# Optimization experiments

Hardware: AMD Instinct MI355X
Metric: run time of the kernel (lower is better)

The kernel has to match this reference:

```python
import jax, jax.numpy as jnp
import numpy as np

N = 50000      # nodes
D = 256        # hid_size (span_emb_size)
DH = D // 2    # per-direction GNN output
V = 2          # num_views = len(retypes)
E = 800000     # edges per view per direction (avg degree 16)


def _gnn(x, edges, W, b):
    """Mean-aggregation GCN message passing: h_dst = relu(mean_{src->dst} x_src @ W + b)."""
    src, dst = edges[0], edges[1]
    msg = x[src] @ W                                   # [E, DH] gather + GEMM
    agg = jax.ops.segment_sum(msg, dst, num_segments=N)
    deg = jax.ops.segment_sum(jnp.ones((msg.shape[0],), x.dtype), dst, num_segments=N)
    return jax.nn.relu(agg / jnp.maximum(deg, 1.0)[:, None] + b)


def setup_inputs() -> dict:
    key = jax.random.key(0)
    ks = jax.random.split(key, 10)
    inps = jax.random.normal(ks[0], (N, D), dtype=jnp.float32)
    fw_edges = jax.random.randint(ks[1], (V, 2, E), 0, N, dtype=jnp.int32)
    bw_edges = jax.random.randint(ks[2], (V, 2, E), 0, N, dtype=jnp.int32)
    s = 1.0 / np.sqrt(D)
    W_fw = jax.random.uniform(ks[3], (V, D, DH), jnp.float32, -s, s)
    b_fw = jax.random.uniform(ks[4], (V, DH), jnp.float32, -s, s)
    W_bw = jax.random.uniform(ks[5], (V, D, DH), jnp.float32, -s, s)
    b_bw = jax.random.uniform(ks[6], (V, DH), jnp.float32, -s, s)
    W1 = jax.random.uniform(ks[7], (D, D), jnp.float32, -s, s)
    b1 = jax.random.uniform(ks[8], (D,), jnp.float32, -s, s)
    return {"inps": inps, "fw_edges": fw_edges, "bw_edges": bw_edges,
            "W_fw": W_fw, "b_fw": b_fw, "W_bw": W_bw, "b_bw": b_bw,
            "W1": W1, "b1": b1}


def reference(inps, fw_edges, bw_edges, W_fw, b_fw, W_bw, b_bw, W1, b1):
    # dropout is identity at inference (p applied only in training)
    acc = jnp.zeros_like(inps)
    for v in range(V):  # small fixed number of structurally distinct views
        fw_o = _gnn(inps, fw_edges[v], W_fw[v], b_fw[v])   # [N, DH]
        bw_o = _gnn(inps, bw_edges[v], W_bw[v], b_bw[v])   # [N, DH]
        acc = acc + jnp.concatenate([bw_o, fw_o], axis=-1)  # [N, D], summed over views
    feats = jax.nn.relu(acc) @ W1 + b1 + inps               # act -> linear1 -> residual
    return feats
```

## Files before the change

kernel.cpp:

```cpp
#include <hip/hip_runtime.h>

#define D_ 256
#define DH_ 128
#define NBMAX 128
#define BCAP 9216

using bf16x8 = __attribute__((ext_vector_type(8))) short;
using f32x4  = __attribute__((ext_vector_type(4))) float;
using f32x2  = __attribute__((ext_vector_type(2))) float;

__device__ __forceinline__ unsigned short f2bf(float f) {
  unsigned int u = __builtin_bit_cast(unsigned int, f);
  u += 0x7fffu + ((u >> 16) & 1u);
  return (unsigned short)(u >> 16);
}
__device__ __forceinline__ unsigned char f2fp8(float f) {
  unsigned int pk = __builtin_amdgcn_cvt_pk_fp8_f32(f, 0.f, 0u, false);
  return (unsigned char)(pk & 0xffu);
}


__global__ __launch_bounds__(512) void part_k(const int* __restrict__ fw,
                                              const int* __restrict__ bw,
                                              int* __restrict__ gcnt,
                                              unsigned int* __restrict__ buckets,
                                              int E_, int nb) {
  __shared__ int hist[NBMAX];
  __shared__ int gbase[NBMAX];
  int g = blockIdx.y;
  const int* src = (g < 2 ? fw : bw) + (size_t)(g & 1) * 2 * E_;
  const int* dst = src + E_;
  int t = threadIdx.x;
  for (int i = t; i < nb; i += 512) hist[i] = 0;
  __syncthreads();
  int base = blockIdx.x * 8192;
  unsigned int pk[16];
  int lp[16];
#pragma unroll
  for (int j = 0; j < 16; ++j) {
    int e = base + j * 512 + t;
    if (e < E_) {
      int s = src[e], d = dst[e];
      pk[j] = (unsigned int)s | ((unsigned int)d << 16);
      lp[j] = atomicAdd(&hist[d >> 9], 1);
    } else {
      pk[j] = 0u; lp[j] = -1;
    }
  }
  __syncthreads();
  for (int i = t; i < nb; i += 512) gbase[i] = atomicAdd(&gcnt[g * NBMAX + i], hist[i]);
  __syncthreads();
#pragma unroll
  for (int j = 0; j < 16; ++j) {
    if (lp[j] >= 0) {
      int b = pk[j] >> 25;
      int pos = gbase[b] + lp[j];
      if (pos < BCAP) buckets[((size_t)(g * NBMAX + b)) * BCAP + pos] = pk[j];
    }
  }
}

__global__ __launch_bounds__(256) void csr_k(const unsigned int* __restrict__ buckets,
                                             const int* __restrict__ gcnt,
                                             int* __restrict__ deg, int* __restrict__ offs,
                                             int* __restrict__ csr, int N_, int E_) {
  __shared__ int ldeg[512];
  __shared__ int loff[512];
  __shared__ int wsum[4];
  __shared__ int red[4];
  int g = blockIdx.y, b = blockIdx.x;
  int t = threadIdx.x;
  int lane = t & 63, w = t >> 6;
  int cnt = min(gcnt[g * NBMAX + b], BCAP);
  const unsigned int* ebuf = buckets + ((size_t)(g * NBMAX + b)) * BCAP;
  int nodebase = b << 9;
  int nloc = min(512, N_ - nodebase);
  for (int i = t; i < 512; i += 256) ldeg[i] = 0;
  int val = (t < b) ? min(gcnt[g * NBMAX + t], BCAP) : 0;
  for (int o = 1; o < 64; o <<= 1) val += __shfl_xor(val, o, 64);
  if (lane == 0) red[w] = val;
  __syncthreads();
  int gb = red[0] + red[1] + red[2] + red[3];
  for (int i = t; i < cnt; i += 256) atomicAdd(&ldeg[(ebuf[i] >> 16) & 511], 1);
  __syncthreads();
  int i0 = w * 128 + lane * 2;
  int a0 = ldeg[i0], a1 = ldeg[i0 + 1];
  int pair = a0 + a1, incl = pair;
  for (int o = 1; o < 64; o <<= 1) {
    int x = __shfl_up(incl, o, 64);
    if (lane >= o) incl += x;
  }
  if (lane == 63) wsum[w] = incl;
  __syncthreads();
  int wpre = 0;
  for (int k = 0; k < w; ++k) wpre += wsum[k];
  int e0 = wpre + incl - pair;
  loff[i0] = e0;
  loff[i0 + 1] = e0 + a0;
  __syncthreads();
  for (int i = t; i < nloc; i += 256) {
    deg[(size_t)g * N_ + nodebase + i] = ldeg[i];
    offs[(size_t)g * N_ + nodebase + i] = gb + loff[i];
  }
  for (int i = t; i < 512; i += 256) ldeg[i] = 0;
  __syncthreads();
  int* csrg = csr + (size_t)g * E_ + gb;
  for (int i = t; i < cnt; i += 256) {
    unsigned int pk = ebuf[i];
    int d = (pk >> 16) & 511;
    int lp = atomicAdd(&ldeg[d], 1);
    csrg[loff[d] + lp] = (int)(pk & 0xffffu);
  }
}


__global__ void prepw_k(const float* __restrict__ Wfw, const float* __restrict__ Wbw,
                        const float* __restrict__ W1,
                        unsigned short* __restrict__ Wt, unsigned short* __restrict__ W1t,
                        int* __restrict__ gcnt) {
  int i = blockIdx.x * blockDim.x + threadIdx.x;
  if (i < 4 * NBMAX) gcnt[i] = 0;
  const int nw = 4 * D_ * DH_;
  if (i < nw) {
    int g = i >> 15;
    int r = i & 32767;
    int n = r >> 8, k = r & 255;
    const float* W = (g < 2 ? Wfw : Wbw) + (size_t)(g & 1) * D_ * DH_;
    Wt[i] = f2bf(W[k * DH_ + n]);
  } else if (i < nw + D_ * D_) {
    int r = i - nw;
    int c = r >> 8, k = r & 255;
    W1t[r] = f2bf(W1[k * D_ + c]);
  }
}


__global__ __launch_bounds__(512, 4) void ygemm_k(const float* __restrict__ x,
                                                  const unsigned short* __restrict__ Wt,
                                                  unsigned char* __restrict__ y, int N_) {
  __shared__ unsigned short At[64 * 256];
  int t = threadIdx.x, lane = t & 63, w = t >> 6;
  int tile = blockIdx.x;
#pragma unroll
  for (int it = 0; it < 8; ++it) {
    int idx = it * 512 + t;
    int row = idx >> 6, slot = idx & 63;
    int gr = tile * 64 + row;
    float4 v = {0.f, 0.f, 0.f, 0.f};
    if (gr < N_) v = ((const float4*)x)[(size_t)gr * 64 + slot];
    int c = slot * 4;
    int sc2 = (c & 7) | ((((c >> 3)) ^ (row & 7)) << 3);
    ushort4 o;
    o.x = f2bf(v.x); o.y = f2bf(v.y); o.z = f2bf(v.z); o.w = f2bf(v.w);
    *(ushort4*)&At[row * 256 + sc2] = o;
  }
  __syncthreads();
  int krow = (lane >> 4) * 8;
  int l15 = lane & 15;
  int g = w >> 1, ch = w & 1;
  const unsigned short* Wg = Wt + (size_t)g * (DH_ * D_);
  f32x4 acc[4][4];
#pragma unroll
  for (int a = 0; a < 4; ++a)
#pragma unroll
    for (int b = 0; b < 4; ++b) acc[a][b] = (f32x4){0.f, 0.f, 0.f, 0.f};
#pragma unroll
  for (int kk = 0; kk < 8; ++kk) {
    bf16x8 bfr[4];
#pragma unroll
    for (int ct = 0; ct < 4; ++ct) {
      int n = ch * 64 + ct * 16 + l15;
      bfr[ct] = *(const bf16x8*)(Wg + (size_t)n * 256 + kk * 32 + krow);
    }
    bf16x8 afr[4];
#pragma unroll
    for (int rt = 0; rt < 4; ++rt) {
      int r = rt * 16 + l15;
      int cc = kk * 32 + krow;
      afr[rt] = *(const bf16x8*)&At[r * 256 + (cc ^ ((r & 7) << 3))];
    }
#pragma unroll
    for (int ct = 0; ct < 4; ++ct)
#pragma unroll
      for (int rt = 0; rt < 4; ++rt)
        acc[rt][ct] = __builtin_amdgcn_mfma_f32_16x16x32_bf16(afr[rt], bfr[ct], acc[rt][ct], 0, 0, 0);
  }
  unsigned char* yg = y + (size_t)g * N_ * DH_;
#pragma unroll
  for (int rt = 0; rt < 4; ++rt)
#pragma unroll
    for (int j = 0; j < 4; ++j) {
      int row = tile * 64 + rt * 16 + (lane >> 4) * 4 + j;
      if (row < N_) {
#pragma unroll
        for (int ct = 0; ct < 4; ++ct)
          yg[(size_t)row * DH_ + ch * 64 + ct * 16 + l15] = f2fp8(acc[rt][ct][j]);
      }
    }
}


__device__ __forceinline__ void acc2(f32x2* s, uint2 q) {
  s[0] += __builtin_amdgcn_cvt_pk_f32_fp8(q.x, false);
  s[1] += __builtin_amdgcn_cvt_pk_f32_fp8(q.x, true);
  s[2] += __builtin_amdgcn_cvt_pk_f32_fp8(q.y, false);
  s[3] += __builtin_amdgcn_cvt_pk_f32_fp8(q.y, true);
}

#define GATHER(sacc, dgv, offv, gidx)                                                   \
  {                                                                                     \
    const int* lst = csr + (size_t)(gidx) * E_ + (offv);                                \
    const unsigned char* yg = y + (size_t)(gidx) * N_ * DH_;                            \
    int jend = (dgv) & ~3;                                                              \
    int j = 0;                                                                          \
    _Pragma("unroll 1")                                                                 \
    for (; j < jend; j += 4) {                                                          \
      int4 iv = *(const int4*)(lst + j);                                                \
      uint2 q0 = *(const uint2*)(yg + ((((unsigned)iv.x & 0xffffu) << 7) + boff));      \
      uint2 q1 = *(const uint2*)(yg + ((((unsigned)iv.y & 0xffffu) << 7) + boff));      \
      uint2 q2 = *(const uint2*)(yg + ((((unsigned)iv.z & 0xffffu) << 7) + boff));      \
      uint2 q3 = *(const uint2*)(yg + ((((unsigned)iv.w & 0xffffu) << 7) + boff));      \
      acc2(sacc, q0); acc2(sacc, q1); acc2(sacc, q2); acc2(sacc, q3);                   \
    }                                                                                   \
    if (j < (dgv)) {                                                                    \
      int4 iv = *(const int4*)(lst + j);                                                \
      uint2 q0 = *(const uint2*)(yg + ((((unsigned)iv.x & 0xffffu) << 7) + boff));      \
      uint2 q1 = *(const uint2*)(yg + ((((unsigned)iv.y & 0xffffu) << 7) + boff));      \
      uint2 q2 = *(const uint2*)(yg + ((((unsigned)iv.z & 0xffffu) << 7) + boff));      \
      if (j + 0 < (dgv)) acc2(sacc, q0);                                                \
      if (j + 1 < (dgv)) acc2(sacc, q1);                                                \
      if (j + 2 < (dgv)) acc2(sacc, q2);                                                \
    }                                                                                   \
  }

__global__ __launch_bounds__(256, 6) void gnn2_k(
    const unsigned char* __restrict__ y,
    const int* __restrict__ deg, const int* __restrict__ offs, const int* __restrict__ csr,
    const float* __restrict__ bias_fw, const float* __restrict__ bias_bw,
    unsigned short* __restrict__ accb, int N_, int E_) {
  const int tid = threadIdx.x;
  const int lane = tid & 63, w = tid >> 6;
  const int grp = lane >> 4, l15 = lane & 15;
  const int tile = blockIdx.x, dir = blockIdx.y;
  const int colbase = dir ? 0 : 128;
  const float* bias = dir ? bias_bw : bias_fw;
  const unsigned boff = l15 * 8;
  const int g0 = dir * 2, g1 = g0 + 1;

#pragma unroll 1
  for (int rr = 0; rr < 2; ++rr) {
    int nd = tile * 32 + rr * 16 + w * 4 + grp;
    bool act = nd < N_;
    int nds = act ? nd : 0;
    f32x2 s0[4], s1[4];
#pragma unroll
    for (int k = 0; k < 4; ++k) { s0[k] = (f32x2){0.f, 0.f}; s1[k] = (f32x2){0.f, 0.f}; }
    int dg0 = deg[(size_t)g0 * N_ + nds];
    int off0 = offs[(size_t)g0 * N_ + nds];
    int dg1 = deg[(size_t)g1 * N_ + nds];
    int off1 = offs[(size_t)g1 * N_ + nds];
    if (!act) { dg0 = 0; dg1 = 0; }

    GATHER(s0, dg0, off0, g0);
    GATHER(s1, dg1, off1, g1);

    float sc0 = 1.0f / (float)max(dg0, 1);
    float sc1 = 1.0f / (float)max(dg1, 1);
    const float* bp0 = bias + boff;
    const float* bp1 = bias + DH_ + boff;
    uint4 pk;
    unsigned* pw = (unsigned*)&pk;
#pragma unroll
    for (int k = 0; k < 4; ++k) {
      float h0 = fmaxf(s0[k].x * sc0 + bp0[2 * k],     0.f) + fmaxf(s1[k].x * sc1 + bp1[2 * k],     0.f);
      float h1 = fmaxf(s0[k].y * sc0 + bp0[2 * k + 1], 0.f) + fmaxf(s1[k].y * sc1 + bp1[2 * k + 1], 0.f);
      pw[k] = (unsigned)f2bf(h0) | ((unsigned)f2bf(h1) << 16);
    }
    if (act) *(uint4*)(accb + (size_t)nd * 256 + colbase + boff) = pk;
  }
}


__global__ __launch_bounds__(512, 4) void gemm2_k(
    const unsigned short* __restrict__ accb, const unsigned short* __restrict__ W1t,
    const float* __restrict__ b1, const float* __restrict__ x,
    float* __restrict__ out, int N_) {
  __shared__ unsigned short Bt[64 * 256];
  int tid = threadIdx.x;
  int lane = tid & 63, w = tid >> 6;
  int l15 = lane & 15;
  int tile = blockIdx.x;
#pragma unroll
  for (int it = 0; it < 4; ++it) {
    int idx = it * 512 + tid;
    int row = idx >> 5, slot = idx & 31;
    int gr = min(tile * 64 + row, N_ - 1);
    uint4 v = *(const uint4*)(accb + (size_t)gr * 256 + slot * 8);
    int c = slot * 8;
    *(uint4*)&Bt[row * 256 + (c ^ ((row & 7) << 3))] = v;
  }
  __syncthreads();
  f32x4 acc[4][2];
#pragma unroll
  for (int a = 0; a < 4; ++a)
#pragma unroll
    for (int b = 0; b < 2; ++b) acc[a][b] = (f32x4){0.f, 0.f, 0.f, 0.f};
  int krow = (lane >> 4) * 8;
#pragma unroll
  for (int kk = 0; kk < 8; ++kk) {
    bf16x8 bfr[2];
#pragma unroll
    for (int ct = 0; ct < 2; ++ct) {
      int cn = w * 32 + ct * 16 + l15;
      bfr[ct] = *(const bf16x8*)(W1t + (size_t)cn * 256 + kk * 32 + krow);
    }
    bf16x8 afr[4];
#pragma unroll
    for (int rt = 0; rt < 4; ++rt) {
      int r = rt * 16 + l15;
      int cc = kk * 32 + krow;
      afr[rt] = *(const bf16x8*)&Bt[r * 256 + (cc ^ ((r & 7) << 3))];
    }
#pragma unroll
    for (int ct = 0; ct < 2; ++ct)
#pragma unroll
      for (int rt = 0; rt < 4; ++rt)
        acc[rt][ct] = __builtin_amdgcn_mfma_f32_16x16x32_bf16(afr[rt], bfr[ct], acc[rt][ct], 0, 0, 0);
  }
#pragma unroll
  for (int ct = 0; ct < 2; ++ct) {
    int col = w * 32 + ct * 16 + l15;
    float bb = b1[col];
#pragma unroll
    for (int rt = 0; rt < 4; ++rt)
#pragma unroll
      for (int j = 0; j < 4; ++j) {
        int row = tile * 64 + rt * 16 + (lane >> 4) * 4 + j;
        if (row < N_)
          out[(size_t)row * 256 + col] = acc[rt][ct][j] + bb + x[(size_t)row * 256 + col];
      }
  }
}


extern "C" void kernel_launch(void* const* d_in, const int* in_sizes, int n_in,
                              void* d_out, int out_size, void* d_ws, size_t ws_size,
                              hipStream_t stream) {
  const float* inps = (const float*)d_in[0];
  const int* fw = (const int*)d_in[1];
  const int* bw = (const int*)d_in[2];
  const float* Wfw = (const float*)d_in[3];
  const float* bfw = (const float*)d_in[4];
  const float* Wbw = (const float*)d_in[5];
  const float* bbw = (const float*)d_in[6];
  const float* W1 = (const float*)d_in[7];
  const float* b1 = (const float*)d_in[8];
  float* out = (float*)d_out;

  int N_ = in_sizes[0] / D_;
  int E_ = in_sizes[1] / 4;
  int nb = (N_ + 511) >> 9;

  char* ws = (char*)d_ws;
  size_t p = 0;
  int* deg = (int*)(ws + p);              p += (size_t)4 * N_ * 4;
  int* offs = (int*)(ws + p);             p += (size_t)4 * N_ * 4;
  int* gcnt = (int*)(ws + p);             p += (size_t)4 * NBMAX * 4;
  int* csr = (int*)(ws + p);              p += (size_t)4 * E_ * 4;
  unsigned int* buckets = (unsigned int*)(ws + p);  p += (size_t)4 * NBMAX * BCAP * 4;
  unsigned short* Wt = (unsigned short*)(ws + p);   p += (size_t)4 * D_ * DH_ * 2;
  unsigned short* W1t = (unsigned short*)(ws + p);  p += (size_t)D_ * D_ * 2;
  unsigned char* y = (unsigned char*)(ws + p);      p += (size_t)4 * N_ * DH_;
  unsigned short* accb = (unsigned short*)(ws + p); p += (size_t)N_ * D_ * 2;

  prepw_k<<<768, 256, 0, stream>>>(Wfw, Wbw, W1, Wt, W1t, gcnt);

  int ntiles64 = (N_ + 63) / 64;
  ygemm_k<<<ntiles64, 512, 0, stream>>>(inps, Wt, y, N_);

  dim3 pgrid((E_ + 8191) / 8192, 4);
  part_k<<<pgrid, 512, 0, stream>>>(fw, bw, gcnt, buckets, E_, nb);
  dim3 cgrid(nb, 4);
  csr_k<<<cgrid, 256, 0, stream>>>(buckets, gcnt, deg, offs, csr, N_, E_);

  int ntiles32 = (N_ + 31) / 32;
  dim3 ggrid(ntiles32, 2);
  gnn2_k<<<ggrid, 256, 0, stream>>>(y, deg, offs, csr, bfw, bbw, accb, N_, E_);
  gemm2_k<<<ntiles64, 512, 0, stream>>>(accb, W1t, b1, inps, out, N_);
}
```

Before: 213.5 us.

## Use per-wave histograms in partition and widen CSR build blocks

The partition kernel now keeps a separate shared-memory histogram per wavefront, which spreads LDS atomic contention across waves. Each bucket's global base is then split into per-wave offsets with a small serial prefix. The CSR build kernel runs 512 threads per block, one thread per local node, which simplifies the scan and adds parallelism for a grid of only 4*nb blocks. The GNN aggregation kernel's launch bounds ask for 8 blocks per CU instead of 6, which may force register spilling.

```diff
diff --git a/kernel.cpp b/kernel.cpp
--- a/kernel.cpp
+++ b/kernel.cpp
@@ -25,13 +25,12 @@
                                               int* __restrict__ gcnt,
                                               unsigned int* __restrict__ buckets,
                                               int E_, int nb) {
-  __shared__ int hist[NBMAX];
-  __shared__ int gbase[NBMAX];
+  __shared__ int hist[8][NBMAX];
   int g = blockIdx.y;
   const int* src = (g < 2 ? fw : bw) + (size_t)(g & 1) * 2 * E_;
   const int* dst = src + E_;
-  int t = threadIdx.x;
-  for (int i = t; i < nb; i += 512) hist[i] = 0;
+  int t = threadIdx.x, w = t >> 6;
+  for (int i = t; i < 8 * NBMAX; i += 512) ((int*)hist)[i] = 0;
   __syncthreads();
   int base = blockIdx.x * 8192;
   unsigned int pk[16];
@@ -42,32 +41,40 @@
     if (e < E_) {
       int s = src[e], d = dst[e];
       pk[j] = (unsigned int)s | ((unsigned int)d << 16);
-      lp[j] = atomicAdd(&hist[d >> 9], 1);
+      lp[j] = atomicAdd(&hist[w][d >> 9], 1);
     } else {
       pk[j] = 0u; lp[j] = -1;
     }
   }
   __syncthreads();
-  for (int i = t; i < nb; i += 512) gbase[i] = atomicAdd(&gcnt[g * NBMAX + i], hist[i]);
+  if (t < nb) {
+    int tot = 0;
+#pragma unroll
+    for (int ww = 0; ww < 8; ++ww) tot += hist[ww][t];
+    int gb = atomicAdd(&gcnt[g * NBMAX + t], tot);
+    int run = gb;
+#pragma unroll
+    for (int ww = 0; ww < 8; ++ww) { int h = hist[ww][t]; hist[ww][t] = run; run += h; }
+  }
   __syncthreads();
 #pragma unroll
   for (int j = 0; j < 16; ++j) {
     if (lp[j] >= 0) {
       int b = pk[j] >> 25;
-      int pos = gbase[b] + lp[j];
+      int pos = hist[w][b] + lp[j];
       if (pos < BCAP) buckets[((size_t)(g * NBMAX + b)) * BCAP + pos] = pk[j];
     }
   }
 }
 
-__global__ __launch_bounds__(256) void csr_k(const unsigned int* __restrict__ buckets,
+__global__ __launch_bounds__(512) void csr_k(const unsigned int* __restrict__ buckets,
                                              const int* __restrict__ gcnt,
                                              int* __restrict__ deg, int* __restrict__ offs,
                                              int* __restrict__ csr, int N_, int E_) {
   __shared__ int ldeg[512];
   __shared__ int loff[512];
-  __shared__ int wsum[4];
-  __shared__ int red[4];
+  __shared__ int wsum[8];
+  __shared__ int red[8];
   int g = blockIdx.y, b = blockIdx.x;
   int t = threadIdx.x;
   int lane = t & 63, w = t >> 6;
@@ -75,17 +82,18 @@
   const unsigned int* ebuf = buckets + ((size_t)(g * NBMAX + b)) * BCAP;
   int nodebase = b << 9;
   int nloc = min(512, N_ - nodebase);
-  for (int i = t; i < 512; i += 256) ldeg[i] = 0;
+  ldeg[t] = 0;
   int val = (t < b) ? min(gcnt[g * NBMAX + t], BCAP) : 0;
   for (int o = 1; o < 64; o <<= 1) val += __shfl_xor(val, o, 64);
   if (lane == 0) red[w] = val;
   __syncthreads();
-  int gb = red[0] + red[1] + red[2] + red[3];
-  for (int i = t; i < cnt; i += 256) atomicAdd(&ldeg[(ebuf[i] >> 16) & 511], 1);
-  __syncthreads();
-  int i0 = w * 128 + lane * 2;
-  int a0 = ldeg[i0], a1 = ldeg[i0 + 1];
-  int pair = a0 + a1, incl = pair;
+  int gb = 0;
+#pragma unroll
+  for (int k = 0; k < 8; ++k) gb += red[k];
+  for (int i = t; i < cnt; i += 512) atomicAdd(&ldeg[(ebuf[i] >> 16) & 511], 1);
+  __syncthreads();
+  int a0 = ldeg[t];
+  int incl = a0;
   for (int o = 1; o < 64; o <<= 1) {
     int x = __shfl_up(incl, o, 64);
     if (lane >= o) incl += x;
@@ -94,18 +102,16 @@
   __syncthreads();
   int wpre = 0;
   for (int k = 0; k < w; ++k) wpre += wsum[k];
-  int e0 = wpre + incl - pair;
-  loff[i0] = e0;
-  loff[i0 + 1] = e0 + a0;
-  __syncthreads();
-  for (int i = t; i < nloc; i += 256) {
-    deg[(size_t)g * N_ + nodebase + i] = ldeg[i];
-    offs[(size_t)g * N_ + nodebase + i] = gb + loff[i];
-  }
-  for (int i = t; i < 512; i += 256) ldeg[i] = 0;
+  loff[t] = wpre + incl - a0;
+  __syncthreads();
+  if (t < nloc) {
+    deg[(size_t)g * N_ + nodebase + t] = ldeg[t];
+    offs[(size_t)g * N_ + nodebase + t] = gb + loff[t];
+  }
+  ldeg[t] = 0;
   __syncthreads();
   int* csrg = csr + (size_t)g * E_ + gb;
-  for (int i = t; i < cnt; i += 256) {
+  for (int i = t; i < cnt; i += 512) {
     unsigned int pk = ebuf[i];
     int d = (pk >> 16) & 511;
     int lp = atomicAdd(&ldeg[d], 1);
@@ -233,7 +239,7 @@
     }                                                                                   \
   }
 
-__global__ __launch_bounds__(256, 6) void gnn2_k(
+__global__ __launch_bounds__(256, 8) void gnn2_k(
     const unsigned char* __restrict__ y,
     const int* __restrict__ deg, const int* __restrict__ offs, const int* __restrict__ csr,
     const float* __restrict__ bias_fw, const float* __restrict__ bias_bw,
@@ -381,7 +387,7 @@
   dim3 pgrid((E_ + 8191) / 8192, 4);
   part_k<<<pgrid, 512, 0, stream>>>(fw, bw, gcnt, buckets, E_, nb);
   dim3 cgrid(nb, 4);
-  csr_k<<<cgrid, 256, 0, stream>>>(buckets, gcnt, deg, offs, csr, N_, E_);
+  csr_k<<<cgrid, 512, 0, stream>>>(buckets, gcnt, deg, offs, csr, N_, E_);
 
   int ntiles32 = (N_ + 31) / 32;
   dim3 ggrid(ntiles32, 2);
```

Result: no change. 215.8 us (+1.1%).
